# Kernel tuning notes

Hardware: AMD Instinct MI355X
Metric: run time of the kernel (lower is better)

Reference implementation:

```python
import jax, jax.numpy as jnp
import numpy as np
from jax import lax

# dims: input features 512, channels 32, seq 256, model dim 256, d_inner 512, d_state 32, dt_rank 16
D_IN = 512; CH = 32; L = 256; DIM = 256; DI = 512; N = 32; DTR = 16; CC = 16; B = 8

def setup_inputs() -> dict:
    key = jax.random.key(0)
    ks = iter(jax.random.split(key, 48))
    def rn(shape, s=0.02):
        return jax.random.normal(next(ks), shape, jnp.float32) * s
    return {
        "x": jax.random.normal(next(ks), (B, CH, L, D_IN), jnp.float32),
        "lin0_w": rn((DIM, D_IN * CH)), "lin0_b": jnp.zeros(DIM),
        "ln0_g": jnp.ones(DIM), "ln0_b": jnp.zeros(DIM),
        "lin1_w": rn((DIM, DIM)), "lin1_b": jnp.zeros(DIM),
        "ln1_g": jnp.ones(DIM), "ln1_b": jnp.zeros(DIM),
        "pos": rn((1, L, DIM)),
        "m_in_w": rn((2 * DI, DIM)),
        "m_conv_w": rn((DI, 1, 4), 0.1), "m_conv_b": jnp.zeros(DI),
        "m_xproj_w": rn((DTR + 2 * N, DI)),
        "m_dt_w": rn((DI, DTR), 0.1), "m_dt_b": jnp.full((DI,), -4.0),
        "m_Alog": jnp.log(jnp.broadcast_to(jnp.arange(1, N + 1, dtype=jnp.float32), (DI, N))),
        "m_D": jnp.ones(DI),
        "m_out_w": rn((DIM, DI)),
        "blk_out_w": rn((DIM, DIM)), "blk_out_b": jnp.zeros(DIM),
        "dec_w": rn((DIM, 2 * DIM)), "dec_b": jnp.zeros(DIM),
        "c1_w": rn((CC, 1, 3, 3), 0.1), "c1_b": jnp.zeros(CC),
        "c2_w": rn((CC, CC, 3, 3), 0.1), "c2_b": jnp.zeros(CC),
        "c3_w": rn((CC, CC, 3, 3), 0.1), "c3_b": jnp.zeros(CC),
        "c4_w": rn((1, CC, 1, 1), 0.1), "c4_b": jnp.zeros(1),
    }

def layernorm(x, g, b):
    mu = jnp.mean(x, -1, keepdims=True)
    var = jnp.var(x, -1, keepdims=True)
    return (x - mu) * lax.rsqrt(var + 1e-5) * g + b

def conv2d(x, w, b):
    y = lax.conv_general_dilated(x, w, (1, 1), 'SAME', dimension_numbers=('NCHW', 'OIHW', 'NCHW'))
    return y + b[None, :, None, None]

def selective_scan(u, dt, A, Bm, Cm, D):
    # u, dt: [B,L,DI]; A: [DI,N]; Bm, Cm: [B,L,N]
    dA = jnp.exp(jnp.einsum('bld,dn->bldn', dt, A))          # [B,L,DI,N]
    dBu = jnp.einsum('bld,bln,bld->bldn', dt, Bm, u)          # [B,L,DI,N]
    def step(h, inp):
        dA_t, dBu_t, C_t = inp
        h = dA_t * h + dBu_t                                  # [B,DI,N]
        y = jnp.einsum('bdn,bn->bd', h, C_t)
        return h, y
    h0 = jnp.zeros((u.shape[0], u.shape[2], A.shape[1]), u.dtype)
    _, ys = lax.scan(step, h0, (jnp.swapaxes(dA, 0, 1), jnp.swapaxes(dBu, 0, 1), jnp.swapaxes(Cm, 0, 1)))
    return jnp.swapaxes(ys, 0, 1) + u * D                     # [B,L,DI]

def mamba(x, m_in_w, m_conv_w, m_conv_b, m_xproj_w, m_dt_w, m_dt_b, m_Alog, m_D, m_out_w):
    Lx = x.shape[1]
    xz = x @ m_in_w.T                                         # [B,L,2*DI]
    xc, z = jnp.split(xz, 2, axis=-1)
    # causal depthwise conv1d, kernel 4, left-pad 3, truncate to L
    xc = jnp.swapaxes(xc, 1, 2)                               # [B,DI,L]
    xc = jnp.pad(xc, ((0, 0), (0, 0), (3, 0)))
    xc = lax.conv_general_dilated(xc, m_conv_w, (1,), 'VALID',
                                  dimension_numbers=('NCH', 'OIH', 'NCH'),
                                  feature_group_count=DI) + m_conv_b[None, :, None]
    xc = jax.nn.silu(jnp.swapaxes(xc[..., :Lx], 1, 2))        # [B,L,DI]
    x_dbl = xc @ m_xproj_w.T                                  # [B,L,DTR+2N]
    dt, Bm, Cm = jnp.split(x_dbl, [DTR, DTR + N], axis=-1)
    dt = jax.nn.softplus(dt @ m_dt_w.T + m_dt_b)              # [B,L,DI]
    A = -jnp.exp(m_Alog)                                      # [DI,N]
    y = selective_scan(xc, dt, A, Bm, Cm, m_D)
    y = y * jax.nn.silu(z)
    return y @ m_out_w.T                                      # [B,L,DIM]

def _forward(x, lin0_w, lin0_b, ln0_g, ln0_b, lin1_w, lin1_b, ln1_g, ln1_b, pos,
             m_in_w, m_conv_w, m_conv_b, m_xproj_w, m_dt_w, m_dt_b, m_Alog, m_D, m_out_w,
             blk_out_w, blk_out_b, dec_w, dec_b,
             c1_w, c1_b, c2_w, c2_b, c3_w, c3_b, c4_w, c4_b):
    b = x.shape[0]
    # encode: [B,CH,L,F] -> permute(0,2,3,1) -> [B,L,F,CH] -> [B,L,F*CH]
    xt = jnp.transpose(x, (0, 2, 3, 1)).reshape(b, L, -1)
    xt = layernorm(jax.nn.relu(xt @ lin0_w.T + lin0_b), ln0_g, ln0_b)
    xt = layernorm(jax.nn.relu(xt @ lin1_w.T + lin1_b), ln1_g, ln1_b)
    skip = xt
    # sequence model
    xs = xt + pos[:, :L, :]
    xs = mamba(xs, m_in_w, m_conv_w, m_conv_b, m_xproj_w, m_dt_w, m_dt_b, m_Alog, m_D, m_out_w)
    xs = xs @ blk_out_w.T + blk_out_b
    # decode
    xd = jnp.concatenate([xs, skip], axis=-1)                 # [B,L,2*DIM]
    xd = jax.nn.relu(xd @ dec_w.T + dec_b)                    # [B,L,DIM]; L*DIM = 256^2
    xd = xd.reshape(b, 1, 256, 256)
    xd = jax.nn.relu(conv2d(xd, c1_w, c1_b))
    xd = jax.nn.relu(conv2d(xd, c2_w, c2_b))
    xd = jax.nn.relu(conv2d(xd, c3_w, c3_b))
    # bilinear 256->128, align_corners=False == exact 2x2 mean pooling
    xd = xd.reshape(b, CC, 128, 2, 128, 2).mean(axis=(3, 5))
    return conv2d(xd, c4_w, c4_b)                             # [B,1,128,128]

def reference(x, lin0_w, lin0_b, ln0_g, ln0_b, lin1_w, lin1_b, ln1_g, ln1_b, pos,
              m_in_w, m_conv_w, m_conv_b, m_xproj_w, m_dt_w, m_dt_b, m_Alog, m_D, m_out_w,
              blk_out_w, blk_out_b, dec_w, dec_b,
              c1_w, c1_b, c2_w, c2_b, c3_w, c3_b, c4_w, c4_b):
    return _forward(x, lin0_w, lin0_b, ln0_g, ln0_b, lin1_w, lin1_b, ln1_g, ln1_b, pos,
                    m_in_w, m_conv_w, m_conv_b, m_xproj_w, m_dt_w, m_dt_b, m_Alog, m_D, m_out_w,
                    blk_out_w, blk_out_b, dec_w, dec_b,
                    c1_w, c1_b, c2_w, c2_b, c3_w, c3_b, c4_w, c4_b)
```

## Files before the change

### kernel.cpp

```cpp
#include <hip/hip_runtime.h>
#include <hip/hip_bf16.h>
#include <cstddef>
#include <cstdint>

#define MROWS 2048
#define KBIG  16384

typedef __attribute__((ext_vector_type(8))) short short8v;
typedef __attribute__((ext_vector_type(4))) float f32x4;
typedef unsigned int u32;

static const size_t F_XT0  = 0;
static const size_t F_SKIP = 524288;
static const size_t F_XS   = 1048576;
static const size_t F_XZ   = 1572864;
static const size_t F_XC   = 3670016;
static const size_t F_XDBL = 4718592;
static const size_t F_DT   = 4882432;
static const size_t F_YG   = 5931008;
static const size_t F_XS2  = 7503872;
static const size_t F_DEC  = 9076736;
static const size_t F_WMED = 9700000;
static const size_t F_WT0  = 10485760;
static const size_t F_PART = 14680064;
static const size_t F_WDT  = 23068672;
static const size_t F_C1   = 10485760;
static const size_t F_C2   = 0;
static const size_t F_C3   = 14680064;

__device__ __forceinline__ float siluf(float v)     { return v / (1.f + __expf(-v)); }
__device__ __forceinline__ float softplusf(float v) { return v > 20.f ? v : log1pf(__expf(v)); }

__device__ __forceinline__ void split2(float v, short& h, short& l) {
  __hip_bfloat16 hb = __float2bfloat16(v);
  float hf = __bfloat162float(hb);
  __hip_bfloat16 lb = __float2bfloat16(v - hf);
  h = *(short*)&hb; l = *(short*)&lb;
}

__device__ __forceinline__ void glds16(const void* g, void* l) {
  __builtin_amdgcn_global_load_lds((const __attribute__((address_space(1))) u32*)g,
                                   (__attribute__((address_space(3))) u32*)l, 16, 0, 0);
}

#define MFMA3(acc, ah, al, bh, bl)                                            \
  acc = __builtin_amdgcn_mfma_f32_16x16x32_bf16(ah, bh, acc, 0, 0, 0);        \
  acc = __builtin_amdgcn_mfma_f32_16x16x32_bf16(al, bh, acc, 0, 0, 0);        \
  acc = __builtin_amdgcn_mfma_f32_16x16x32_bf16(ah, bl, acc, 0, 0, 0);

__device__ __forceinline__ void med_tile_blk(const float* w, unsigned short* th,
                                             unsigned short* tl, int K, int nslots, int b) {
  int slot = b * 256 + threadIdx.x;
  if (slot >= nslots) return;
  int NS = K >> 5;
  int col = slot & 127, kg = (slot >> 7) & 3, rest = slot >> 9;
  int s = rest % NS, nt = rest / NS;
  const float* src = w + (size_t)(nt * 128 + col) * K + (s << 5) + (kg << 3);
  short8v h8, l8;
#pragma unroll
  for (int j = 0; j < 8; ++j) {
    short hh, ll; split2(src[j], hh, ll);
    h8[j] = hh; l8[j] = ll;
  }
  *(short8v*)(th + (size_t)slot * 8) = h8;
  *(short8v*)(tl + (size_t)slot * 8) = l8;
}

__device__ __forceinline__ void conv_tile_blk(const float* w, unsigned short* th,
                                              unsigned short* tl, int b) {
  int slot = b * 256 + threadIdx.x;
  if (slot >= 320) return;
  int oc = slot & 15;
  int sfq = slot >> 4;
  int s = sfq >> 2, fq = sfq & 3;
  short8v h8, l8;
#pragma unroll
  for (int j = 0; j < 8; ++j) {
    int k = s * 32 + fq * 8 + j;
    float v = 0.f;
    if (k < 144) {
      int dydx = k >> 4, ic = k & 15;
      v = w[oc * 144 + ic * 9 + dydx];
    }
    short hh, ll; split2(v, hh, ll);
    h8[j] = hh; l8[j] = ll;
  }
  *(short8v*)(th + (size_t)slot * 8) = h8;
  *(short8v*)(tl + (size_t)slot * 8) = l8;
}

__device__ __forceinline__ void wdtbc_tile_blk(const float* dtw, const float* xpw,
                                               unsigned short* th, unsigned short* tl, int b) {
  int slot = b * 256 + threadIdx.x;
  int col = slot & 127, kg = (slot >> 7) & 3, rest = slot >> 9;
  int s = rest & 15, nt = rest >> 4;
  int d = nt * 128 + col;
  short8v h8, l8;
  if (d < 512) {
    float wrow[16];
#pragma unroll
    for (int r = 0; r < 16; ++r) wrow[r] = dtw[d * 16 + r];
#pragma unroll
    for (int j = 0; j < 8; ++j) {
      int k = s * 32 + kg * 8 + j;
      float v = 0.f;
#pragma unroll
      for (int r = 0; r < 16; ++r) v = fmaf(wrow[r], xpw[r * 512 + k], v);
      short hh, ll; split2(v, hh, ll);
      h8[j] = hh; l8[j] = ll;
    }
  } else {
#pragma unroll
    for (int j = 0; j < 8; ++j) {
      int k = s * 32 + kg * 8 + j;
      float v = (d < 576) ? xpw[(size_t)(d - 512 + 16) * 512 + k] : 0.f;
      short hh, ll; split2(v, hh, ll);
      h8[j] = hh; l8[j] = ll;
    }
  }
  *(short8v*)(th + (size_t)slot * 8) = h8;
  *(short8v*)(tl + (size_t)slot * 8) = l8;
}

__global__ __launch_bounds__(256) void tile_all(const float* __restrict__ lin0_w,
                                                unsigned short* __restrict__ wt0h,
                                                unsigned short* __restrict__ wt0l,
                                                unsigned short* __restrict__ wmed,
                                                const float* __restrict__ m_in_w,
                                                const float* __restrict__ lin1_w,
                                                const float* __restrict__ m_out_w,
                                                const float* __restrict__ blk_w,
                                                const float* __restrict__ dec_w,
                                                const float* __restrict__ c2_w,
                                                const float* __restrict__ c3_w,
                                                const float* __restrict__ m_dt_w,
                                                const float* __restrict__ m_xproj_w,
                                                unsigned short* __restrict__ wdth,
                                                unsigned short* __restrict__ wdtl,
                                                unsigned short* __restrict__ w2h,
                                                unsigned short* __restrict__ w2l) {
  __shared__ float ls[32 * 264];
  int b = blockIdx.x;
  int tid = threadIdx.x;
  if (b < 512) {
    int ct = b >> 6, kt = b & 63;
    int c0 = ct << 5, k0 = kt << 8;
    for (int u = tid; u < 2048; u += 256) {
      int col_l = u >> 6, f4i = u & 63;
      int k_l = f4i << 2;
      float4 v = *(const float4*)(lin0_w + (size_t)(c0 + col_l) * KBIG + k0 + k_l);
      float vv[4] = {v.x, v.y, v.z, v.w};
#pragma unroll
      for (int j = 0; j < 4; ++j) {
        int idx = k_l + j;
        ls[col_l * 264 + idx + (idx >> 5)] = vv[j];
      }
    }
    __syncthreads();
    for (int oi = tid; oi < 1024; oi += 256) {
      int col_l = oi & 31, c = oi >> 5;
      short8v h8, l8;
#pragma unroll
      for (int j = 0; j < 8; ++j) {
        float v = ls[col_l * 264 + j * 33 + c];
        short hh, ll; split2(v, hh, ll);
        h8[j] = hh; l8[j] = ll;
      }
      size_t slot = ((size_t)(c * 64 + kt)) * 256 + c0 + col_l;
      *(short8v*)(wt0h + slot * 8) = h8;
      *(short8v*)(wt0l + slot * 8) = l8;
    }
    return;
  }
  b -= 512;
  if (b < 128) { med_tile_blk(m_in_w,  wmed,           wmed + 262144,  256, 32768, b); return; }
  b -= 128;
  if (b < 32)  { med_tile_blk(lin1_w,  wmed + 524288,  wmed + 589824,  256, 8192,  b); return; }
  b -= 32;
  if (b < 64)  { med_tile_blk(dec_w,   wmed + 1048576, wmed + 1179648, 512, 16384, b); return; }
  b -= 64;
  if (b < 2)   { conv_tile_blk(c2_w, wmed + 1310720, wmed + 1313280, b); return; }
  b -= 2;
  if (b < 2)   { conv_tile_blk(c3_w, wmed + 1315840, wmed + 1318400, b); return; }
  b -= 2;
  if (b < 160) { wdtbc_tile_blk(m_dt_w, m_xproj_w, wdth, wdtl, b); return; }
  b -= 160;
  {
    int slot = b * 256 + tid;
    int col = slot & 127, kg = (slot >> 7) & 3, rest = slot >> 9;
    int s = rest & 15, nt = rest >> 4;
    int kb2 = s * 32 + ((b & 1) << 4);
    float acc[8];
#pragma unroll
    for (int j = 0; j < 8; ++j) acc[j] = 0.f;
    float* ows = ls + 4224;
    for (int r0 = 0; r0 < 256; r0 += 32) {
      __syncthreads();
      for (int idx = tid; idx < 4096; idx += 256) {
        int dl = idx >> 5, rr = idx & 31;
        ls[dl * 33 + rr] = blk_w[(size_t)(nt * 128 + dl) * 256 + r0 + rr];
      }
      for (int idx = tid; idx < 512; idx += 256) {
        int rr = idx >> 4, kk = idx & 15;
        ows[rr * 16 + kk] = m_out_w[(size_t)(r0 + rr) * 512 + kb2 + kk];
      }
      __syncthreads();
#pragma unroll 4
      for (int rr = 0; rr < 32; ++rr) {
        float bv = ls[col * 33 + rr];
        const float* op = &ows[rr * 16 + ((kg & 1) << 3)];
#pragma unroll
        for (int j = 0; j < 8; ++j) acc[j] = fmaf(bv, op[j], acc[j]);
      }
    }
    short8v h8, l8;
#pragma unroll
    for (int j = 0; j < 8; ++j) {
      short hh, ll; split2(acc[j], hh, ll);
      h8[j] = hh; l8[j] = ll;
    }
    *(short8v*)(w2h + (size_t)slot * 8) = h8;
    *(short8v*)(w2l + (size_t)slot * 8) = l8;
  }
}

__global__ __launch_bounds__(512, 2) void lin0_mfma(const float* __restrict__ x,
                                                    const unsigned short* __restrict__ wh,
                                                    const unsigned short* __restrict__ wl,
                                                    float* __restrict__ wsbase) {
  __shared__ short8v Ad[2][2][1024];
  __shared__ short8v Bd[2][2][1024];
  int bid = blockIdx.x;
  int mt = bid >> 5, z = bid & 31;
  int tid = threadIdx.x;
  int lane = tid & 63, wid = tid >> 6;
  int wm = wid >> 2, wn = wid & 3;
  int fi = lane & 15, fq = lane >> 4;
  int arow = tid >> 1, kh = tid & 1;
  const float* xrow = x + (size_t)mt * 4194304 + (size_t)z * 131072 + (size_t)arow * 512;
  int skg = wid & 3, shl = wid >> 2;
  const unsigned short* wsrc = shl ? wl : wh;
  int aoff[8], boff[4];
#pragma unroll
  for (int mi = 0; mi < 8; ++mi) {
    int row = wm * 128 + mi * 16 + fi;
    aoff[mi] = fq * 256 + (row ^ (fq << 2));
  }
#pragma unroll
  for (int ni = 0; ni < 4; ++ni) boff[ni] = fq * 256 + wn * 64 + ni * 16 + fi;

  f32x4 acc[8][4];
#pragma unroll
  for (int mi = 0; mi < 8; ++mi)
#pragma unroll
    for (int ni = 0; ni < 4; ++ni) acc[mi][ni] = (f32x4)(0.f);

  {
    int slotbase = ((z * 16 + 0) * 4 + skg) * 256;
#pragma unroll
    for (int q = 0; q < 4; ++q)
      glds16(wsrc + (size_t)(slotbase + q * 64 + lane) * 8,
             (void*)&Bd[0][shl][skg * 256 + q * 64]);
    int f0 = kh << 4;
    float vv[16];
#pragma unroll
    for (int j4 = 0; j4 < 4; ++j4) {
      float4 v = *(const float4*)(xrow + f0 + 4 * j4);
      vv[4 * j4] = v.x; vv[4 * j4 + 1] = v.y; vv[4 * j4 + 2] = v.z; vv[4 * j4 + 3] = v.w;
    }
#pragma unroll
    for (int jg = 0; jg < 2; ++jg) {
      short8v h8, l8;
#pragma unroll
      for (int j = 0; j < 8; ++j) { short hh, ll; split2(vv[jg * 8 + j], hh, ll); h8[j] = hh; l8[j] = ll; }
      int kg = (kh << 1) + jg;
      int idx = kg * 256 + (arow ^ (kg << 2));
      Ad[0][0][idx] = h8; Ad[0][1][idx] = l8;
    }
    __syncthreads();
  }

  for (int s = 0; s < 16; ++s) {
    int cb = s & 1, nb = cb ^ 1;
    bool more = s < 15;
    float vv[16];
    if (more) {
      int slotbase = ((z * 16 + s + 1) * 4 + skg) * 256;
#pragma unroll
      for (int q = 0; q < 4; ++q)
        glds16(wsrc + (size_t)(slotbase + q * 64 + lane) * 8,
               (void*)&Bd[nb][shl][skg * 256 + q * 64]);
      int f0 = ((s + 1) << 5) + (kh << 4);
#pragma unroll
      for (int j4 = 0; j4 < 4; ++j4) {
        float4 v = *(const float4*)(xrow + f0 + 4 * j4);
        vv[4 * j4] = v.x; vv[4 * j4 + 1] = v.y; vv[4 * j4 + 2] = v.z; vv[4 * j4 + 3] = v.w;
      }
    }
    short8v fah[8], fal[8];
#pragma unroll
    for (int mi = 0; mi < 8; ++mi) { fah[mi] = Ad[cb][0][aoff[mi]]; fal[mi] = Ad[cb][1][aoff[mi]]; }
#pragma unroll
    for (int ni = 0; ni < 4; ++ni) {
      short8v bh = Bd[cb][0][boff[ni]];
      short8v bl = Bd[cb][1][boff[ni]];
#pragma unroll
      for (int mi = 0; mi < 8; ++mi) { MFMA3(acc[mi][ni], fah[mi], fal[mi], bh, bl); }
    }
    if (more) {
#pragma unroll
      for (int jg = 0; jg < 2; ++jg) {
        short8v h8, l8;
#pragma unroll
        for (int j = 0; j < 8; ++j) { short hh, ll; split2(vv[jg * 8 + j], hh, ll); h8[j] = hh; l8[j] = ll; }
        int kg = (kh << 1) + jg;
        int idx = kg * 256 + (arow ^ (kg << 2));
        Ad[nb][0][idx] = h8; Ad[nb][1][idx] = l8;
      }
    }
    __syncthreads();
  }

  size_t slabbase = (z < 16) ? (F_PART + (size_t)z * 524288) : ((size_t)(z - 16) * 524288);
  float* po = wsbase + slabbase + (size_t)mt * 65536;
#pragma unroll
  for (int mi = 0; mi < 8; ++mi)
#pragma unroll
    for (int ni = 0; ni < 4; ++ni) {
      int mloc = wm * 128 + mi * 16 + fq * 4;
      int n = wn * 64 + ni * 16 + fi;
#pragma unroll
      for (int r = 0; r < 4; ++r)
        po[(size_t)(mloc + r) * 256 + n] = acc[mi][ni][r];
    }
}

template <int ACT, int HASBIAS, int SRC2, int DTBC>
__global__ __launch_bounds__(256, 2) void med_mfma(const float* __restrict__ A, int lda,
                                                   const float* __restrict__ A2,
                                                   const unsigned short* __restrict__ wh,
                                                   const unsigned short* __restrict__ wl,
                                                   const float* __restrict__ bias,
                                                   float* __restrict__ out,
                                                   float* __restrict__ bc_out,
                                                   int K, int N) {
  __shared__ short8v Ahs[2][2][256];
  __shared__ short8v Bd[2][2][512];
  int nt = blockIdx.x, mt = blockIdx.y;
  int NS = K >> 5;
  int tid = threadIdx.x;
  int lane = tid & 63, wid = tid >> 6;
  int fi = lane & 15, fq = lane >> 4;
  int arow = tid >> 2, akg = tid & 3;
  int awidx = akg * 64 + (arow ^ (akg << 2));
  int m0 = mt << 6;
  size_t wtbase = (size_t)nt * NS;
  int aoff[4], boff[2];
#pragma unroll
  for (int mi = 0; mi < 4; ++mi) {
    int row = mi * 16 + fi;
    aoff[mi] = fq * 64 + (row ^ (fq << 2));
  }
#pragma unroll
  for (int ni = 0; ni < 2; ++ni) boff[ni] = fq * 128 + wid * 32 + ni * 16 + fi;

  f32x4 acc[4][2];
#pragma unroll
  for (int mi = 0; mi < 4; ++mi)
#pragma unroll
    for (int ni = 0; ni < 2; ++ni) acc[mi][ni] = (f32x4)(0.f);

  {
#pragma unroll
    for (int p = 0; p < 2; ++p) {
      int q = (wid << 1) + p;
      size_t gb = wtbase * 8192 + (size_t)q * 1024 + (size_t)lane * 16;
      glds16((const char*)wh + gb, (char*)&Bd[0][0][0] + q * 1024);
      glds16((const char*)wl + gb, (char*)&Bd[0][1][0] + q * 1024);
    }
    const float* gp = A + (size_t)(m0 + arow) * lda + (akg << 3);
    float4 v0 = *(const float4*)gp, v1 = *(const float4*)(gp + 4);
    float vv[8] = {v0.x, v0.y, v0.z, v0.w, v1.x, v1.y, v1.z, v1.w};
    short8v h8, l8;
#pragma unroll
    for (int j = 0; j < 8; ++j) { short hh, ll; split2(vv[j], hh, ll); h8[j] = hh; l8[j] = ll; }
    Ahs[0][0][awidx] = h8; Ahs[0][1][awidx] = l8;
    __syncthreads();
  }

  for (int s = 0; s < NS; ++s) {
    int cb = s & 1, nb = cb ^ 1;
    bool more = (s + 1) < NS;
    float4 v0, v1;
    if (more) {
#pragma unroll
      for (int p = 0; p < 2; ++p) {
        int q = (wid << 1) + p;
        size_t gb = (wtbase + s + 1) * 8192 + (size_t)q * 1024 + (size_t)lane * 16;
        glds16((const char*)wh + gb, (char*)&Bd[nb][0][0] + q * 1024);
        glds16((const char*)wl + gb, (char*)&Bd[nb][1][0] + q * 1024);
      }
      int sk = (s + 1) << 5;
      const float* gp;
      if (SRC2 && sk >= 256)
        gp = A2 + (size_t)(m0 + arow) * 256 + (sk - 256) + (akg << 3);
      else
        gp = A + (size_t)(m0 + arow) * lda + sk + (akg << 3);
      v0 = *(const float4*)gp; v1 = *(const float4*)(gp + 4);
    }
    short8v fah[4], fal[4];
#pragma unroll
    for (int mi = 0; mi < 4; ++mi) { fah[mi] = Ahs[cb][0][aoff[mi]]; fal[mi] = Ahs[cb][1][aoff[mi]]; }
#pragma unroll
    for (int ni = 0; ni < 2; ++ni) {
      short8v bh = Bd[cb][0][boff[ni]];
      short8v bl = Bd[cb][1][boff[ni]];
#pragma unroll
      for (int mi = 0; mi < 4; ++mi) { MFMA3(acc[mi][ni], fah[mi], fal[mi], bh, bl); }
    }
    if (more) {
      float vv[8] = {v0.x, v0.y, v0.z, v0.w, v1.x, v1.y, v1.z, v1.w};
      short8v h8, l8;
#pragma unroll
      for (int j = 0; j < 8; ++j) { short hh, ll; split2(vv[j], hh, ll); h8[j] = hh; l8[j] = ll; }
      Ahs[nb][0][awidx] = h8; Ahs[nb][1][awidx] = l8;
    }
    __syncthreads();
  }

#pragma unroll
  for (int mi = 0; mi < 4; ++mi)
#pragma unroll
    for (int ni = 0; ni < 2; ++ni) {
      int n = (nt << 7) + wid * 32 + ni * 16 + fi;
#pragma unroll
      for (int r = 0; r < 4; ++r) {
        int m = m0 + mi * 16 + fq * 4 + r;
        float a = acc[mi][ni][r];
        if (DTBC) {
          if (n < 512) out[(size_t)m * 512 + n] = softplusf(a + bias[n]);
          else if (n < 576) bc_out[(size_t)m * 64 + (n - 512)] = a;
        } else {
          float v = a + (HASBIAS ? bias[n] : 0.f);
          if (ACT == 1) v = fmaxf(v, 0.f);
          out[(size_t)m * N + n] = v;
        }
      }
    }
}

__global__ __launch_bounds__(256) void ln32_k(const float* part_a, const float* part_b,
                                              const float* __restrict__ bias,
                                              const float* __restrict__ g,
                                              const float* __restrict__ bb,
                                              float* out) {
  int m = blockIdx.x, t = threadIdx.x;
  float s = bias[t];
  for (int z = 0; z < 16; ++z) s += part_a[((size_t)z * MROWS + m) * 256 + t];
  for (int z = 0; z < 16; ++z) s += part_b[((size_t)z * MROWS + m) * 256 + t];
  float v = fmaxf(s, 0.f);
  float sum = v, sq = v * v;
#pragma unroll
  for (int o = 1; o < 64; o <<= 1) { sum += __shfl_xor(sum, o); sq += __shfl_xor(sq, o); }
  __shared__ float s1[4], s2[4];
  int w = t >> 6;
  if ((t & 63) == 0) { s1[w] = sum; s2[w] = sq; }
  __syncthreads();
  sum = s1[0] + s1[1] + s1[2] + s1[3];
  sq  = s2[0] + s2[1] + s2[2] + s2[3];
  float mu  = sum * (1.f / 256.f);
  float var = sq * (1.f / 256.f) - mu * mu;
  out[(size_t)m * 256 + t] = (v - mu) * rsqrtf(var + 1e-5f) * g[t] + bb[t];
}

__global__ __launch_bounds__(256) void ln_pos_k(const float* __restrict__ part,
                                                const float* __restrict__ bias,
                                                const float* __restrict__ g,
                                                const float* __restrict__ bb,
                                                const float* __restrict__ pos,
                                                float* __restrict__ skip,
                                                float* __restrict__ xs) {
  int m = blockIdx.x, t = threadIdx.x;
  float s = bias[t] + part[(size_t)m * 256 + t];
  float v = fmaxf(s, 0.f);
  float sum = v, sq = v * v;
#pragma unroll
  for (int o = 1; o < 64; o <<= 1) { sum += __shfl_xor(sum, o); sq += __shfl_xor(sq, o); }
  __shared__ float s1[4], s2[4];
  int w = t >> 6;
  if ((t & 63) == 0) { s1[w] = sum; s2[w] = sq; }
  __syncthreads();
  sum = s1[0] + s1[1] + s1[2] + s1[3];
  sq  = s2[0] + s2[1] + s2[2] + s2[3];
  float mu  = sum * (1.f / 256.f);
  float var = sq * (1.f / 256.f) - mu * mu;
  float o2 = (v - mu) * rsqrtf(var + 1e-5f) * g[t] + bb[t];
  skip[(size_t)m * 256 + t] = o2;
  xs[(size_t)m * 256 + t] = o2 + pos[(m & 255) * 256 + t];
}

__global__ __launch_bounds__(256) void conv1d_silu_k(const float* __restrict__ xz,
                                                     const float* __restrict__ w,
                                                     const float* __restrict__ cb,
                                                     float* __restrict__ xc) {
  int i = blockIdx.x * 256 + threadIdx.x;
  int m = i >> 9, d = i & 511;
  int b = m >> 8, l = m & 255;
  float s = cb[d];
#pragma unroll
  for (int j = 0; j < 4; ++j) {
    int ll = l - 3 + j;
    if (ll >= 0) s = fmaf(w[(d << 2) + j], xz[((size_t)((b << 8) + ll) << 10) + d], s);
  }
  xc[(size_t)m * 512 + d] = siluf(s);
}

__global__ __launch_bounds__(256, 1) void scan_k(const float* __restrict__ dt,
                                                 const float* __restrict__ u,
                                                 const float* __restrict__ bc,
                                                 const float* __restrict__ Alog,
                                                 const float* __restrict__ Dp,
                                                 const float* __restrict__ xz,
                                                 float* __restrict__ yg) {
  __shared__ float pbuf[2][4][2][16][33];
  int tid  = threadIdx.x;
  int widx = tid >> 6, lane = tid & 63;
  int wid  = (blockIdx.x << 2) + widx;
  int n = lane & 31, ch = lane >> 5;
  int d0 = (wid & 255) << 1;
  int d = d0 + ch;
  int b = wid >> 8;
  size_t base = (size_t)b << 8;
  float Av = -__expf(Alog[(d << 5) + n]);
  float Dv0 = Dp[d0], Dv1 = Dp[d0 + 1];
  float h = 0.f;
  int row = lane & 31;
  int rch = row >> 4, rlp = row & 15;
  int nh  = lane >> 5;
  int drow = d0 + rch;
  float Dsel = rch ? Dv1 : Dv0;

  for (int w0 = 0; w0 < 256; w0 += 16) {
    int wb = (w0 >> 4) & 1;
    float dA[16], dBu[16], Cv[16];
#pragma unroll
    for (int j = 0; j < 16; ++j) {
      size_t r = base + w0 + j;
      float dtv = dt[(r << 9) + d];
      float uv  = u [(r << 9) + d];
      float Bv  = bc[(r << 6) + n];
      Cv[j]     = bc[(r << 6) + 32 + n];
      dA[j]  = __expf(dtv * Av);
      dBu[j] = dtv * Bv * uv;
    }
#pragma unroll
    for (int j = 0; j < 16; ++j) {
      h = fmaf(dA[j], h, dBu[j]);
      pbuf[wb][widx][ch][j][n] = h * Cv[j];
    }
    __syncthreads();
    float s = 0.f;
#pragma unroll
    for (int nn = 0; nn < 16; ++nn) s += pbuf[wb][widx][rch][rlp][(nh << 4) + nn];
    s += __shfl_xor(s, 32);
    if (lane < 32) {
      size_t r = base + w0 + rlp;
      float uv = u[(r << 9) + drow];
      float zv = xz[(r << 10) + 512 + drow];
      yg[(r << 9) + drow] = (s + uv * Dsel) * siluf(zv);
    }
  }
}

template <int IC>
__global__ __launch_bounds__(256) void conv3x3_k(const float* __restrict__ in,
                                                 const float* __restrict__ w,
                                                 const float* __restrict__ bias,
                                                 float* __restrict__ out) {
  __shared__ float t[IC][6][68];
  __shared__ float wl[IC * 144];
  __shared__ float bl[16];
  int bid = blockIdx.x;
  int x0 = (bid & 3) << 6;
  int y0 = ((bid >> 2) & 63) << 2;
  int bb = bid >> 8;
  int tid = threadIdx.x;
  for (int i = tid; i < IC * 144; i += 256) {
    int oc = i & 15, t2 = i >> 4;
    wl[i] = w[(size_t)oc * (IC * 9) + t2];
  }
  if (tid < 16) bl[tid] = bias[tid];
  for (int i = tid; i < IC * 396; i += 256) {
    int ic = i / 396, rem = i - ic * 396;
    int r = rem / 66, cx = rem - r * 66;
    int y = y0 - 1 + r, xx = x0 - 1 + cx;
    float v = 0.f;
    if (y >= 0 && y < 256 && xx >= 0 && xx < 256)
      v = in[(((size_t)bb * IC + ic) << 16) + (y << 8) + xx];
    t[ic][r][cx] = v;
  }
  __syncthreads();
  int tx = tid & 15, row = (tid >> 4) & 3, ocq = tid >> 6;
  float acc[4][4];
#pragma unroll
  for (int o = 0; o < 4; ++o)
#pragma unroll
    for (int p = 0; p < 4; ++p) acc[o][p] = 0.f;

  for (int ic = 0; ic < IC; ++ic) {
#pragma unroll
    for (int dy = 0; dy < 3; ++dy) {
      const float* rp = &t[ic][row + dy][tx << 2];
      float rv[6];
#pragma unroll
      for (int q = 0; q < 6; ++q) rv[q] = rp[q];
#pragma unroll
      for (int dx = 0; dx < 3; ++dx) {
        const float* wp4 = &wl[(((ic * 3 + dy) * 3 + dx) << 4) + (ocq << 2)];
#pragma unroll
        for (int o = 0; o < 4; ++o) {
          float wv = wp4[o];
#pragma unroll
          for (int p = 0; p < 4; ++p) acc[o][p] = fmaf(rv[p + dx], wv, acc[o][p]);
        }
      }
    }
  }
  int xo = x0 + (tx << 2), yo = y0 + row;
#pragma unroll
  for (int o = 0; o < 4; ++o) {
    int oc = (ocq << 2) + o;
    float4 v4;
    v4.x = fmaxf(acc[o][0] + bl[oc], 0.f);
    v4.y = fmaxf(acc[o][1] + bl[oc], 0.f);
    v4.z = fmaxf(acc[o][2] + bl[oc], 0.f);
    v4.w = fmaxf(acc[o][3] + bl[oc], 0.f);
    *(float4*)&out[(((size_t)bb * 16 + oc) << 16) + (yo << 8) + xo] = v4;
  }
}

__global__ __launch_bounds__(256, 2) void conv_mfma(const float* __restrict__ in,
                                                    const unsigned short* __restrict__ wth,
                                                    const unsigned short* __restrict__ wtl,
                                                    const float* __restrict__ bias,
                                                    float* __restrict__ out) {
  __shared__ __align__(16) char smem[58752];
  unsigned short* inh = (unsigned short*)smem;
  unsigned short* inl = inh + 14688;
  int bid = blockIdx.x;
  int txi = bid & 7;
  int tyi = (bid >> 3) & 15;
  int bb  = bid >> 7;
  int x0 = txi << 5, y0 = tyi << 4;
  int tid = threadIdx.x;

  for (int i = tid; i < 9792; i += 256) {
    int ic = i / 612, rem = i - ic * 612;
    int y = rem / 34, xx = rem - y * 34;
    int gy = y0 + y - 1, gx = x0 + xx - 1;
    float v = 0.f;
    if (gy >= 0 && gy < 256 && gx >= 0 && gx < 256)
      v = in[(((size_t)bb * 16 + ic) << 16) + (gy << 8) + gx];
    short hh, ll; split2(v, hh, ll);
    int a = (y * 34 + xx) * 24 + ic;
    inh[a] = (unsigned short)hh; inl[a] = (unsigned short)ll;
  }
  __syncthreads();

  int lane = tid & 63, w = tid >> 6;
  int fi = lane & 15, fq = lane >> 4;
  int fqh = fq >> 1, ich8 = (fq & 1) << 3;

  int adel[5];
#pragma unroll
  for (int s = 0; s < 5; ++s) {
    int dydx = 2 * s + fqh;
    if (dydx > 8) dydx = 8;
    int dy = dydx / 3, dx = dydx - dy * 3;
    adel[s] = (dy * 34 + dx) * 24;
  }
  int abase[8];
#pragma unroll
  for (int q = 0; q < 8; ++q) {
    int px = ((w * 8 + q) << 4) + fi;
    int y = px >> 5, xx = px & 31;
    abase[q] = (y * 34 + xx) * 24 + ich8;
  }
  short8v bh[5], bl[5];
#pragma unroll
  for (int s = 0; s < 5; ++s) {
    int slot = ((s * 4 + fq) * 16 + fi) * 8;
    bh[s] = *(const short8v*)(wth + slot);
    bl[s] = *(const short8v*)(wtl + slot);
  }

  f32x4 acc[8];
#pragma unroll
  for (int q = 0; q < 8; ++q) acc[q] = (f32x4)(0.f);

#pragma unroll
  for (int s = 0; s < 5; ++s) {
#pragma unroll
    for (int q = 0; q < 8; ++q) {
      short8v ah = *(const short8v*)&inh[abase[q] + adel[s]];
      short8v al = *(const short8v*)&inl[abase[q] + adel[s]];
      MFMA3(acc[q], ah, al, bh[s], bl[s]);
    }
  }
  __syncthreads();

  float* outs = (float*)smem;
#pragma unroll
  for (int q = 0; q < 8; ++q) {
    int pxb = ((w * 8 + q) << 4) + (fq << 2);
#pragma unroll
    for (int r = 0; r < 4; ++r)
      outs[fi * 514 + pxb + r] = acc[q][r];
  }
  __syncthreads();
  for (int i = tid; i < 8192; i += 256) {
    int oc = i >> 9, px = i & 511;
    int y = px >> 5, xx = px & 31;
    float v = fmaxf(outs[oc * 514 + px] + bias[oc], 0.f);
    out[(((size_t)bb * 16 + oc) << 16) + ((y0 + y) << 8) + x0 + xx] = v;
  }
}

__global__ __launch_bounds__(256) void pool_c4_k(const float* __restrict__ in,
                                                 const float* __restrict__ w4,
                                                 const float* __restrict__ b4,
                                                 float* __restrict__ out) {
  int i = blockIdx.x * 256 + threadIdx.x;
  int xq = i & 63, y = (i >> 6) & 127, b = i >> 13;
  float s0 = b4[0], s1 = b4[0];
#pragma unroll
  for (int ic = 0; ic < 16; ++ic) {
    const float* p = in + (((size_t)b * 16 + ic) << 16) + ((size_t)(y << 1) << 8) + (xq << 2);
    float4 a0 = *(const float4*)p;
    float4 a1 = *(const float4*)(p + 256);
    float m0 = 0.25f * (a0.x + a0.y + a1.x + a1.y);
    float m1 = 0.25f * (a0.z + a0.w + a1.z + a1.w);
    float wv = w4[ic];
    s0 = fmaf(wv, m0, s0);
    s1 = fmaf(wv, m1, s1);
  }
  float2 o2 = make_float2(s0, s1);
  *(float2*)&out[(size_t)b * 16384 + y * 128 + (xq << 1)] = o2;
}

extern "C" void kernel_launch(void* const* d_in, const int* in_sizes, int n_in,
                              void* d_out, int out_size, void* d_ws, size_t ws_size,
                              hipStream_t stream) {
  const float* x        = (const float*)d_in[0];
  const float* lin0_w   = (const float*)d_in[1];
  const float* lin0_b   = (const float*)d_in[2];
  const float* ln0_g    = (const float*)d_in[3];
  const float* ln0_bb   = (const float*)d_in[4];
  const float* lin1_w   = (const float*)d_in[5];
  const float* lin1_b   = (const float*)d_in[6];
  const float* ln1_g    = (const float*)d_in[7];
  const float* ln1_bb   = (const float*)d_in[8];
  const float* pos      = (const float*)d_in[9];
  const float* m_in_w   = (const float*)d_in[10];
  const float* m_conv_w = (const float*)d_in[11];
  const float* m_conv_b = (const float*)d_in[12];
  const float* m_xproj_w= (const float*)d_in[13];
  const float* m_dt_w   = (const float*)d_in[14];
  const float* m_dt_b   = (const float*)d_in[15];
  const float* m_Alog   = (const float*)d_in[16];
  const float* m_D      = (const float*)d_in[17];
  const float* m_out_w  = (const float*)d_in[18];
  const float* blk_w    = (const float*)d_in[19];
  const float* blk_b    = (const float*)d_in[20];
  const float* dec_w    = (const float*)d_in[21];
  const float* dec_b    = (const float*)d_in[22];
  const float* c1_w     = (const float*)d_in[23];
  const float* c1_b     = (const float*)d_in[24];
  const float* c2_w     = (const float*)d_in[25];
  const float* c2_b     = (const float*)d_in[26];
  const float* c3_w     = (const float*)d_in[27];
  const float* c3_b     = (const float*)d_in[28];
  const float* c4_w     = (const float*)d_in[29];
  const float* c4_b     = (const float*)d_in[30];

  float* ws  = (float*)d_ws;
  float* out = (float*)d_out;

  unsigned short* wt0h = (unsigned short*)(ws + F_WT0);
  unsigned short* wt0l = wt0h + 4194304;
  unsigned short* wmed = (unsigned short*)(ws + F_WMED);
  unsigned short* inw_h = wmed,           * inw_l = wmed + 262144;
  unsigned short* l1_h  = wmed + 524288,  * l1_l  = wmed + 589824;
  unsigned short* dc_h  = wmed + 1048576, * dc_l  = wmed + 1179648;
  unsigned short* wc2h  = wmed + 1310720, * wc2l  = wmed + 1313280;
  unsigned short* wc3h  = wmed + 1315840, * wc3l  = wmed + 1318400;
  unsigned short* wdth  = (unsigned short*)(ws + F_WDT);
  unsigned short* wdtl  = wdth + 327680;
  unsigned short* w2h   = wdtl + 327680;
  unsigned short* w2l   = w2h + 131072;

  tile_all<<<964, 256, 0, stream>>>(lin0_w, wt0h, wt0l, wmed,
                                    m_in_w, lin1_w, m_out_w, blk_w, dec_w,
                                    c2_w, c3_w, m_dt_w, m_xproj_w,
                                    wdth, wdtl, w2h, w2l);
  lin0_mfma<<<256, 512, 0, stream>>>(x, wt0h, wt0l, ws);
  ln32_k<<<MROWS, 256, 0, stream>>>(ws + F_PART, ws, lin0_b, ln0_g, ln0_bb, ws + F_XT0);
  med_mfma<0, 0, 0, 0><<<dim3(2, 32), 256, 0, stream>>>(ws + F_XT0, 256, nullptr, l1_h, l1_l,
                                                        nullptr, ws + F_PART, nullptr, 256, 256);
  ln_pos_k<<<MROWS, 256, 0, stream>>>(ws + F_PART, lin1_b, ln1_g, ln1_bb, pos,
                                      ws + F_SKIP, ws + F_XS);
  med_mfma<0, 0, 0, 0><<<dim3(8, 32), 256, 0, stream>>>(ws + F_XS, 256, nullptr, inw_h, inw_l,
                                                        nullptr, ws + F_XZ, nullptr, 256, 1024);
  conv1d_silu_k<<<4096, 256, 0, stream>>>(ws + F_XZ, m_conv_w, m_conv_b, ws + F_XC);
  med_mfma<0, 1, 0, 1><<<dim3(5, 32), 256, 0, stream>>>(ws + F_XC, 512, nullptr, wdth, wdtl,
                                                        m_dt_b, ws + F_DT, ws + F_XDBL, 512, 512);
  scan_k<<<512, 256, 0, stream>>>(ws + F_DT, ws + F_XC, ws + F_XDBL, m_Alog, m_D,
                                  ws + F_XZ, ws + F_YG);
  med_mfma<0, 1, 0, 0><<<dim3(2, 32), 256, 0, stream>>>(ws + F_YG, 512, nullptr, w2h, w2l,
                                                        blk_b, ws + F_XS2, nullptr, 512, 256);
  med_mfma<1, 1, 1, 0><<<dim3(2, 32), 256, 0, stream>>>(ws + F_XS2, 256, ws + F_SKIP, dc_h, dc_l,
                                                        dec_b, ws + F_DEC, nullptr, 512, 256);
  conv3x3_k<1><<<2048, 256, 0, stream>>>(ws + F_DEC, c1_w, c1_b, ws + F_C1);
  conv_mfma<<<1024, 256, 0, stream>>>(ws + F_C1, wc2h, wc2l, c2_b, ws + F_C2);
  conv_mfma<<<1024, 256, 0, stream>>>(ws + F_C2, wc3h, wc3l, c3_b, ws + F_C3);
  pool_c4_k<<<256, 256, 0, stream>>>(ws + F_C3, c4_w, c4_b, out);
}
```

Before: 335.4 us.

## Fuse conv1 into conv2 prologue and pool+1x1 conv into conv3 epilogue

Removes the standalone single-channel conv3x3 kernel by recomputing conv1 (with halo) inside the conv2 MFMA kernel's tile-load stage from the decoder output. The final 2x2 mean-pool and 1x1 conv are folded into the conv3 epilogue, so the 16-channel conv3 output is never written to global memory. This cuts two launches and large intermediate global round-trips (C1 and C3 tensors), at the cost of redundant conv1 recompute on halos and extra LDS.

```diff
diff --git a/kernel.cpp b/kernel.cpp
--- a/kernel.cpp
+++ b/kernel.cpp
@@ -24,9 +24,7 @@
 static const size_t F_WT0  = 10485760;
 static const size_t F_PART = 14680064;
 static const size_t F_WDT  = 23068672;
-static const size_t F_C1   = 10485760;
 static const size_t F_C2   = 0;
-static const size_t F_C3   = 14680064;
 
 __device__ __forceinline__ float siluf(float v)     { return v / (1.f + __expf(-v)); }
 __device__ __forceinline__ float softplusf(float v) { return v > 20.f ? v : log1pf(__expf(v)); }
@@ -572,81 +570,20 @@
   }
 }
 
-template <int IC>
-__global__ __launch_bounds__(256) void conv3x3_k(const float* __restrict__ in,
-                                                 const float* __restrict__ w,
-                                                 const float* __restrict__ bias,
-                                                 float* __restrict__ out) {
-  __shared__ float t[IC][6][68];
-  __shared__ float wl[IC * 144];
-  __shared__ float bl[16];
-  int bid = blockIdx.x;
-  int x0 = (bid & 3) << 6;
-  int y0 = ((bid >> 2) & 63) << 2;
-  int bb = bid >> 8;
-  int tid = threadIdx.x;
-  for (int i = tid; i < IC * 144; i += 256) {
-    int oc = i & 15, t2 = i >> 4;
-    wl[i] = w[(size_t)oc * (IC * 9) + t2];
-  }
-  if (tid < 16) bl[tid] = bias[tid];
-  for (int i = tid; i < IC * 396; i += 256) {
-    int ic = i / 396, rem = i - ic * 396;
-    int r = rem / 66, cx = rem - r * 66;
-    int y = y0 - 1 + r, xx = x0 - 1 + cx;
-    float v = 0.f;
-    if (y >= 0 && y < 256 && xx >= 0 && xx < 256)
-      v = in[(((size_t)bb * IC + ic) << 16) + (y << 8) + xx];
-    t[ic][r][cx] = v;
-  }
-  __syncthreads();
-  int tx = tid & 15, row = (tid >> 4) & 3, ocq = tid >> 6;
-  float acc[4][4];
-#pragma unroll
-  for (int o = 0; o < 4; ++o)
-#pragma unroll
-    for (int p = 0; p < 4; ++p) acc[o][p] = 0.f;
-
-  for (int ic = 0; ic < IC; ++ic) {
-#pragma unroll
-    for (int dy = 0; dy < 3; ++dy) {
-      const float* rp = &t[ic][row + dy][tx << 2];
-      float rv[6];
-#pragma unroll
-      for (int q = 0; q < 6; ++q) rv[q] = rp[q];
-#pragma unroll
-      for (int dx = 0; dx < 3; ++dx) {
-        const float* wp4 = &wl[(((ic * 3 + dy) * 3 + dx) << 4) + (ocq << 2)];
-#pragma unroll
-        for (int o = 0; o < 4; ++o) {
-          float wv = wp4[o];
-#pragma unroll
-          for (int p = 0; p < 4; ++p) acc[o][p] = fmaf(rv[p + dx], wv, acc[o][p]);
-        }
-      }
-    }
-  }
-  int xo = x0 + (tx << 2), yo = y0 + row;
-#pragma unroll
-  for (int o = 0; o < 4; ++o) {
-    int oc = (ocq << 2) + o;
-    float4 v4;
-    v4.x = fmaxf(acc[o][0] + bl[oc], 0.f);
-    v4.y = fmaxf(acc[o][1] + bl[oc], 0.f);
-    v4.z = fmaxf(acc[o][2] + bl[oc], 0.f);
-    v4.w = fmaxf(acc[o][3] + bl[oc], 0.f);
-    *(float4*)&out[(((size_t)bb * 16 + oc) << 16) + (yo << 8) + xo] = v4;
-  }
-}
-
+template <int FUSE1, int POOL>
 __global__ __launch_bounds__(256, 2) void conv_mfma(const float* __restrict__ in,
                                                     const unsigned short* __restrict__ wth,
                                                     const unsigned short* __restrict__ wtl,
                                                     const float* __restrict__ bias,
-                                                    float* __restrict__ out) {
-  __shared__ __align__(16) char smem[58752];
+                                                    float* __restrict__ out,
+                                                    const float* __restrict__ c1w,
+                                                    const float* __restrict__ c1b,
+                                                    const float* __restrict__ w4,
+                                                    const float* __restrict__ b4) {
+  __shared__ __align__(16) char smem[61632];
   unsigned short* inh = (unsigned short*)smem;
   unsigned short* inl = inh + 14688;
+  float* decs = (float*)(smem + 58752);
   int bid = blockIdx.x;
   int txi = bid & 7;
   int tyi = (bid >> 3) & 15;
@@ -654,16 +591,46 @@
   int x0 = txi << 5, y0 = tyi << 4;
   int tid = threadIdx.x;
 
-  for (int i = tid; i < 9792; i += 256) {
-    int ic = i / 612, rem = i - ic * 612;
-    int y = rem / 34, xx = rem - y * 34;
-    int gy = y0 + y - 1, gx = x0 + xx - 1;
-    float v = 0.f;
-    if (gy >= 0 && gy < 256 && gx >= 0 && gx < 256)
-      v = in[(((size_t)bb * 16 + ic) << 16) + (gy << 8) + gx];
-    short hh, ll; split2(v, hh, ll);
-    int a = (y * 34 + xx) * 24 + ic;
-    inh[a] = (unsigned short)hh; inl[a] = (unsigned short)ll;
+  if (FUSE1) {
+    for (int i = tid; i < 720; i += 256) {
+      int a = i / 36, c = i - a * 36;
+      int gy = y0 + a - 2, gx = x0 + c - 2;
+      float v = 0.f;
+      if (gy >= 0 && gy < 256 && gx >= 0 && gx < 256)
+        v = in[(size_t)bb * 65536 + (gy << 8) + gx];
+      decs[i] = v;
+    }
+    __syncthreads();
+    for (int i = tid; i < 9792; i += 256) {
+      int ic = i / 612, rem = i - ic * 612;
+      int y = rem / 34, xx = rem - y * 34;
+      int gy = y0 + y - 1, gx = x0 + xx - 1;
+      float v = 0.f;
+      if (gy >= 0 && gy < 256 && gx >= 0 && gx < 256) {
+        float acc = 0.f;
+#pragma unroll
+        for (int dy = 0; dy < 3; ++dy)
+#pragma unroll
+          for (int dx = 0; dx < 3; ++dx)
+            acc = fmaf(c1w[ic * 9 + dy * 3 + dx], decs[(y + dy) * 36 + xx + dx], acc);
+        v = fmaxf(acc + c1b[ic], 0.f);
+      }
+      short hh, ll; split2(v, hh, ll);
+      int a = (y * 34 + xx) * 24 + ic;
+      inh[a] = (unsigned short)hh; inl[a] = (unsigned short)ll;
+    }
+  } else {
+    for (int i = tid; i < 9792; i += 256) {
+      int ic = i / 612, rem = i - ic * 612;
+      int y = rem / 34, xx = rem - y * 34;
+      int gy = y0 + y - 1, gx = x0 + xx - 1;
+      float v = 0.f;
+      if (gy >= 0 && gy < 256 && gx >= 0 && gx < 256)
+        v = in[(((size_t)bb * 16 + ic) << 16) + (gy << 8) + gx];
+      short hh, ll; split2(v, hh, ll);
+      int a = (y * 34 + xx) * 24 + ic;
+      inh[a] = (unsigned short)hh; inl[a] = (unsigned short)ll;
+    }
   }
   __syncthreads();
 
@@ -718,34 +685,31 @@
       outs[fi * 514 + pxb + r] = acc[q][r];
   }
   __syncthreads();
-  for (int i = tid; i < 8192; i += 256) {
-    int oc = i >> 9, px = i & 511;
-    int y = px >> 5, xx = px & 31;
-    float v = fmaxf(outs[oc * 514 + px] + bias[oc], 0.f);
-    out[(((size_t)bb * 16 + oc) << 16) + ((y0 + y) << 8) + x0 + xx] = v;
-  }
-}
-
-__global__ __launch_bounds__(256) void pool_c4_k(const float* __restrict__ in,
-                                                 const float* __restrict__ w4,
-                                                 const float* __restrict__ b4,
-                                                 float* __restrict__ out) {
-  int i = blockIdx.x * 256 + threadIdx.x;
-  int xq = i & 63, y = (i >> 6) & 127, b = i >> 13;
-  float s0 = b4[0], s1 = b4[0];
-#pragma unroll
-  for (int ic = 0; ic < 16; ++ic) {
-    const float* p = in + (((size_t)b * 16 + ic) << 16) + ((size_t)(y << 1) << 8) + (xq << 2);
-    float4 a0 = *(const float4*)p;
-    float4 a1 = *(const float4*)(p + 256);
-    float m0 = 0.25f * (a0.x + a0.y + a1.x + a1.y);
-    float m1 = 0.25f * (a0.z + a0.w + a1.z + a1.w);
-    float wv = w4[ic];
-    s0 = fmaf(wv, m0, s0);
-    s1 = fmaf(wv, m1, s1);
-  }
-  float2 o2 = make_float2(s0, s1);
-  *(float2*)&out[(size_t)b * 16384 + y * 128 + (xq << 1)] = o2;
+  if (POOL) {
+    if (tid < 128) {
+      int py = tid >> 4, pxx = tid & 15;
+      float s = b4[0];
+#pragma unroll
+      for (int ic = 0; ic < 16; ++ic) {
+        float vb = bias[ic];
+        int base = ic * 514 + (py << 6) + (pxx << 1);
+        float v00 = fmaxf(outs[base]      + vb, 0.f);
+        float v01 = fmaxf(outs[base + 1]  + vb, 0.f);
+        float v10 = fmaxf(outs[base + 32] + vb, 0.f);
+        float v11 = fmaxf(outs[base + 33] + vb, 0.f);
+        float m4 = 0.25f * (v00 + v01 + v10 + v11);
+        s = fmaf(w4[ic], m4, s);
+      }
+      out[(size_t)bb * 16384 + ((y0 >> 1) + py) * 128 + (x0 >> 1) + pxx] = s;
+    }
+  } else {
+    for (int i = tid; i < 8192; i += 256) {
+      int oc = i >> 9, px = i & 511;
+      int y = px >> 5, xx = px & 31;
+      float v = fmaxf(outs[oc * 514 + px] + bias[oc], 0.f);
+      out[(((size_t)bb * 16 + oc) << 16) + ((y0 + y) << 8) + x0 + xx] = v;
+    }
+  }
 }
 
 extern "C" void kernel_launch(void* const* d_in, const int* in_sizes, int n_in,
@@ -820,8 +784,8 @@
                                                         blk_b, ws + F_XS2, nullptr, 512, 256);
   med_mfma<1, 1, 1, 0><<<dim3(2, 32), 256, 0, stream>>>(ws + F_XS2, 256, ws + F_SKIP, dc_h, dc_l,
                                                         dec_b, ws + F_DEC, nullptr, 512, 256);
-  conv3x3_k<1><<<2048, 256, 0, stream>>>(ws + F_DEC, c1_w, c1_b, ws + F_C1);
-  conv_mfma<<<1024, 256, 0, stream>>>(ws + F_C1, wc2h, wc2l, c2_b, ws + F_C2);
-  conv_mfma<<<1024, 256, 0, stream>>>(ws + F_C2, wc3h, wc3l, c3_b, ws + F_C3);
-  pool_c4_k<<<256, 256, 0, stream>>>(ws + F_C3, c4_w, c4_b, out);
-}
+  conv_mfma<1, 0><<<1024, 256, 0, stream>>>(ws + F_DEC, wc2h, wc2l, c2_b, ws + F_C2,
+                                            c1_w, c1_b, nullptr, nullptr);
+  conv_mfma<0, 1><<<1024, 256, 0, stream>>>(ws + F_C2, wc3h, wc3l, c3_b, out,
+                                            nullptr, nullptr, c4_w, c4_b);
+}
```

After: 304.5 us. 9.2% less time.
